# Optimization experiments

Hardware: AMD Instinct MI355X
Metric: run time of the kernel (lower is better)

Reference implementation:

```python
import jax, jax.numpy as jnp
import numpy as np
from jax.ops import segment_sum, segment_max

B, P, NP, EP = 128, 16, 256, 1280
EPG, ODIM, NH = 2048, 256, 128
EPS = 1e-5


def _bn(x, g, b):
    # BatchNorm1d (training-mode batch statistics), biased variance like torch
    mu = x.mean(0)
    var = ((x - mu) ** 2).mean(0)
    return g * (x - mu) * jax.lax.rsqrt(var + EPS) + b


def _gat(feat, src, dst, W, al, ar, resW, bias):
    # DGL GATConv: fc -> per-head attn logits -> leaky_relu -> edge softmax over dst -> aggregate; + residual fc + bias
    n = feat.shape[0]
    H, D = al.shape
    z = (feat @ W).reshape(n, H, D)
    el = (z * al).sum(-1)                                  # [n,H]
    er = (z * ar).sum(-1)
    e = jax.nn.leaky_relu(el[src] + er[dst], 0.2)          # [E,H]
    m = segment_max(e, dst, num_segments=n)
    ex = jnp.exp(e - m[dst])
    s = segment_sum(ex, dst, num_segments=n)
    a = ex / (s[dst] + 1e-9)
    rst = segment_sum(a[:, :, None] * z[src], dst, num_segments=n)  # [n,H,D]
    res = (feat @ resW).reshape(n, H, D)
    return (rst + res + bias.reshape(1, H, D)).reshape(n, H * D)


def _plane(feat, src, dst, p):
    # PlaneGraphEncoder forward (eval: dropout off)
    h = _gat(feat, src, dst, p['W1'], p['al1'], p['ar1'], p['res1'], p['b1'])
    h = jax.nn.relu(_bn(h, p['g1'], p['be1']))
    h = _gat(h, src, dst, p['W2'], p['al2'], p['ar2'], p['res2'], p['b2'])
    h = jax.nn.relu(_bn(h, p['g2'], p['be2']))
    rep = h.mean(0)                                        # dgl.mean_nodes -> [32]
    d = jax.nn.relu(_bn(h @ p['dW1'] + p['db1'], p['dg'], p['dbe']))
    recon = d @ p['dW2'] + p['db2']                        # [n,1]
    rloss = jnp.mean((recon - feat) ** 2)
    return rep, rloss


def _masked_gc(h, src, dst, mask_f, W, b):
    # DGL GraphConv(norm='both') with edge_weight = mask[src]*mask[dst]; structural degrees, clamp>=1
    n = h.shape[0]
    ones = jnp.ones(src.shape[0], h.dtype)
    d_out = jnp.maximum(segment_sum(ones, src, num_segments=n), 1.0)
    d_in = jnp.maximum(segment_sum(ones, dst, num_segments=n), 1.0)
    ew = mask_f[src] * mask_f[dst]                         # [E]
    hs = h * jax.lax.rsqrt(d_out)[:, None]
    agg = segment_sum(ew[:, None] * hs[src], dst, num_segments=n)
    return (agg * jax.lax.rsqrt(d_in)[:, None]) @ W + b


def _forward(plane_feat, original_features,
             W1, al1, ar1, res1, b1, g1, be1,
             W2, al2, ar2, res2, b2, g2, be2,
             dW1, db1, dg, dbe, dW2, db2,
             ft_W, ft_b, ft_g, ft_be, gc_W, gc_b, gbn_g, gbn_be,
             c1_W, c1_b, ln_g, ln_be, c2_W, c2_b,
             plane_src, plane_dst, patient_src, patient_dst, mask):
    pp = dict(W1=W1, al1=al1, ar1=ar1, res1=res1, b1=b1, g1=g1, be1=be1,
              W2=W2, al2=al2, ar2=ar2, res2=res2, b2=b2, g2=g2, be2=be2,
              dW1=dW1, db1=db1, dg=dg, dbe=dbe, dW2=dW2, db2=db2)
    enc_b = jax.vmap(_plane, in_axes=(0, 0, 0, None))      # over patients
    enc_pb = jax.vmap(enc_b, in_axes=(1, 1, 1, 0))         # over planes (params axis 0)
    reps, rlosses = enc_pb(plane_feat, plane_src, plane_dst, pp)   # [P,B,32], [P,B]
    plane_rep = jnp.transpose(reps, (1, 0, 2)).reshape(plane_feat.shape[0], -1)  # [B, P*32]
    avg_recon = rlosses.mean()                             # sum / (B*P)

    x = jnp.concatenate([original_features, plane_rep], axis=1)   # [B, fused]
    h = jax.nn.relu(_bn(x @ ft_W + ft_b, ft_g, ft_be))
    mask_f = mask.astype(h.dtype)
    h_sum = h
    for i in range(3):
        hn = _masked_gc(h, patient_src, patient_dst, mask_f, gc_W[i], gc_b[i])
        hn = jax.nn.relu(_bn(hn, gbn_g[i], gbn_be[i]))
        h = hn + h
        h_sum = h_sum + h
    h = h_sum / 4.0                                        # mean over [h0,h1,h2,h3]

    z = h @ c1_W + c1_b
    mu = z.mean(-1, keepdims=True)
    var = ((z - mu) ** 2).mean(-1, keepdims=True)
    z = jax.nn.relu(ln_g * (z - mu) * jax.lax.rsqrt(var + EPS) + ln_be)
    logits = z @ c2_W + c2_b
    return logits, avg_recon


def setup_inputs() -> dict:
    key = jax.random.key(0)
    ks = iter(jax.random.split(key, 64))
    f = lambda shape, s=0.1: jax.random.normal(next(ks), shape, jnp.float32) * s
    inp = dict(
        plane_feat=f((B, P, NP, 1), 1.0),
        plane_src=jax.random.randint(next(ks), (B, P, EP), 0, NP, jnp.int32),
        plane_dst=jax.random.randint(next(ks), (B, P, EP), 0, NP, jnp.int32),
        patient_src=jax.random.randint(next(ks), (EPG,), 0, B, jnp.int32),
        patient_dst=jax.random.randint(next(ks), (EPG,), 0, B, jnp.int32),
        original_features=f((B, ODIM), 1.0),
        mask=jax.random.randint(next(ks), (B,), 0, 2, jnp.int32),
        # per-plane encoder params, stacked over P
        W1=f((P, 1, 128)), al1=f((P, 2, 64)), ar1=f((P, 2, 64)),
        res1=f((P, 1, 128)), b1=f((P, 128)),
        g1=jnp.ones((P, 128)), be1=jnp.zeros((P, 128)),
        W2=f((P, 128, 32)), al2=f((P, 1, 32)), ar2=f((P, 1, 32)),
        res2=f((P, 128, 32)), b2=f((P, 32)),
        g2=jnp.ones((P, 32)), be2=jnp.zeros((P, 32)),
        dW1=f((P, 32, 128)), db1=f((P, 128)),
        dg=jnp.ones((P, 128)), dbe=jnp.zeros((P, 128)),
        dW2=f((P, 128, 1)), db2=f((P, 1)),
        # patient-level params
        ft_W=f((ODIM + P * 32, NH)), ft_b=f((NH,)),
        ft_g=jnp.ones((NH,)), ft_be=jnp.zeros((NH,)),
        gc_W=f((3, NH, NH)), gc_b=f((3, NH)),
        gbn_g=jnp.ones((3, NH)), gbn_be=jnp.zeros((3, NH)),
        c1_W=f((NH, NH // 2)), c1_b=f((NH // 2,)),
        ln_g=jnp.ones((NH // 2,)), ln_be=jnp.zeros((NH // 2,)),
        c2_W=f((NH // 2, 2)), c2_b=f((2,)),
    )
    return inp


def reference(plane_feat, plane_src, plane_dst, patient_src, patient_dst,
              original_features, mask,
              W1, al1, ar1, res1, b1, g1, be1,
              W2, al2, ar2, res2, b2, g2, be2,
              dW1, db1, dg, dbe, dW2, db2,
              ft_W, ft_b, ft_g, ft_be, gc_W, gc_b, gbn_g, gbn_be,
              c1_W, c1_b, ln_g, ln_be, c2_W, c2_b):
    return _forward(plane_feat, original_features,
                    W1, al1, ar1, res1, b1, g1, be1,
                    W2, al2, ar2, res2, b2, g2, be2,
                    dW1, db1, dg, dbe, dW2, db2,
                    ft_W, ft_b, ft_g, ft_be, gc_W, gc_b, gbn_g, gbn_be,
                    c1_W, c1_b, ln_g, ln_be, c2_W, c2_b,
                    plane_src, plane_dst, patient_src, patient_dst, mask)
```

## Files before the change

### kernel.cpp

```cpp
#include <hip/hip_runtime.h>

#define B_    128
#define P_    16
#define NP_   256
#define EP_   1280
#define EPG_  2048
#define ODIM_ 256
#define NH_   128

typedef __attribute__((ext_vector_type(8))) short s8_t;
typedef __attribute__((ext_vector_type(4))) short s4_t;
typedef __attribute__((ext_vector_type(4))) float f4_t;

__device__ __forceinline__ unsigned short f2b(float x) {
  unsigned u = __builtin_bit_cast(unsigned, x);
  u = (u + 0x7fffu + ((u >> 16) & 1u)) >> 16;
  return (unsigned short)u;
}
__device__ __forceinline__ float b2f(short x) {
  unsigned u = ((unsigned)(unsigned short)x) << 16;
  return __builtin_bit_cast(float, u);
}

struct SmemA {
  float f[256];
  union {
    __align__(16) unsigned short wT1[64 * 136];
    __align__(16) unsigned short z2[256 * 40];
  } u1;
  __align__(16) unsigned short dW1T[128 * 36];
  union {
    struct { float S0a[256]; float S1a[256]; } a;
    float redf[512];
  } u2;
  float el2[256], er2[256];
  union {
    struct { float abg0[128], abg1[128], abg2[128]; } a;
    struct { float al2v[32], ar2v[32], dW2v[128]; } b;
  } u3;
  union {
    int cnt[256];
    struct { float scA[32], shA[32], dscA[64], dshA[64]; } b;
  } u4;
  unsigned short esrc[1280];
  int wtot[4];
  float r8[4][8]; float stat[8]; float wA[2], wB[2];
  float rlacc;
};

__global__ __launch_bounds__(256, 3) void plane_enc(
    const float* __restrict__ feat, const int* __restrict__ esrcg, const int* __restrict__ edstg,
    const float* __restrict__ W1, const float* __restrict__ al1, const float* __restrict__ ar1,
    const float* __restrict__ res1, const float* __restrict__ b1, const float* __restrict__ g1,
    const float* __restrict__ be1,
    const float* __restrict__ W2, const float* __restrict__ al2, const float* __restrict__ ar2,
    const float* __restrict__ res2, const float* __restrict__ g2, const float* __restrict__ be2,
    const float* __restrict__ dW1, const float* __restrict__ dg, const float* __restrict__ dbe,
    const float* __restrict__ dW2, const float* __restrict__ db2,
    float* __restrict__ rep_out, float* __restrict__ rlp_out)
{
  __shared__ SmemA s;
  const int g = blockIdx.x;
  const int p = g & 15;
  const int t = threadIdx.x;
  const int lane = t & 63, wv = t >> 6;
  const int l15 = lane & 15, quad = lane >> 4;

  s.f[t] = feat[g * NP_ + t];
  if (t == 0) s.rlacc = 0.f;
  s.u4.cnt[t] = 0;
  __syncthreads();

  const int* gs = esrcg + g * EP_;
  const int* gd = edstg + g * EP_;
  for (int k = t; k < EP_; k += 256) atomicAdd(&s.u4.cnt[gd[k]], 1);
  __syncthreads();
  int v = s.u4.cnt[t];
  int incl = v;
  #pragma unroll
  for (int off = 1; off < 64; off <<= 1) {
    int n = __shfl_up(incl, off, 64);
    if (lane >= off) incl += n;
  }
  if (lane == 63) s.wtot[wv] = incl;
  __syncthreads();
  int woff = 0;
  for (int w = 0; w < wv; w++) woff += s.wtot[w];
  const int myStart = woff + incl - v;
  const int myDeg = v;
  __syncthreads();
  s.u4.cnt[t] = myStart;
  __syncthreads();
  for (int k = t; k < EP_; k += 256) {
    int d = gd[k];
    int pos = atomicAdd(&s.u4.cnt[d], 1);
    s.esrc[pos] = (unsigned short)gs[k];
  }
  {
    const float* W2g = W2 + p * 4096;
    const float* Rg  = res2 + p * 4096;
    for (int q = 0; q < 16; q++) {
      int idx = t + 256 * q;
      int k = idx >> 5, n = idx & 31;
      s.u1.wT1[n * 136 + k]        = f2b(W2g[idx]);
      s.u1.wT1[(n + 32) * 136 + k] = f2b(Rg[idx]);
    }
  }
  if (t < 128) {
    float w1v = W1[p * 128 + t];
    s.el2[t] = w1v * al1[p * 128 + t];
    s.er2[t] = w1v * ar1[p * 128 + t];
  }
  __syncthreads();
  if (t < 2) {
    float a = 0.f, bq = 0.f;
    for (int d2 = 0; d2 < 64; d2++) { a += s.el2[t * 64 + d2]; bq += s.er2[t * 64 + d2]; }
    s.wA[t] = a; s.wB[t] = bq;
  }
  __syncthreads();

  const float fi = s.f[t];
  float S0, S1;
  {
    const float wa0 = s.wA[0], wb0 = s.wB[0], wa1 = s.wA[1], wb1 = s.wB[1];
    float m0 = -1e30f, m1 = -1e30f;
    for (int j = 0; j < myDeg; j++) {
      float fs = s.f[s.esrc[myStart + j]];
      float e0 = wa0 * fs + wb0 * fi; e0 = e0 > 0.f ? e0 : 0.2f * e0;
      float e1 = wa1 * fs + wb1 * fi; e1 = e1 > 0.f ? e1 : 0.2f * e1;
      m0 = fmaxf(m0, e0); m1 = fmaxf(m1, e1);
    }
    float ss0 = 0.f, ss1 = 0.f, U0 = 0.f, U1 = 0.f;
    for (int j = 0; j < myDeg; j++) {
      float fs = s.f[s.esrc[myStart + j]];
      float e0 = wa0 * fs + wb0 * fi; e0 = e0 > 0.f ? e0 : 0.2f * e0;
      float e1 = wa1 * fs + wb1 * fi; e1 = e1 > 0.f ? e1 : 0.2f * e1;
      float x0 = __expf(e0 - m0), x1 = __expf(e1 - m1);
      ss0 += x0; U0 += x0 * fs;
      ss1 += x1; U1 += x1 * fs;
    }
    S0 = U0 / (ss0 + 1e-9f);
    S1 = U1 / (ss1 + 1e-9f);
    s.u2.a.S0a[t] = S0; s.u2.a.S1a[t] = S1;
  }

  {
    float vals[8] = {fi, fi * fi, S0, S0 * S0, S0 * fi, S1, S1 * S1, S1 * fi};
    #pragma unroll
    for (int d2 = 32; d2 > 0; d2 >>= 1) {
      #pragma unroll
      for (int q = 0; q < 8; q++) vals[q] += __shfl_down(vals[q], d2, 64);
    }
    if (lane == 0) {
      #pragma unroll
      for (int q = 0; q < 8; q++) s.r8[wv][q] = vals[q];
    }
  }
  __syncthreads();
  if (t < 8) s.stat[t] = (s.r8[0][t] + s.r8[1][t] + s.r8[2][t] + s.r8[3][t]) * (1.f / 256.f);
  __syncthreads();
  if (t < 128) {
    float mf = s.stat[0], ef2 = s.stat[1];
    int hh = t >> 6;
    float mS = s.stat[2 + 3 * hh], eS2 = s.stat[3 + 3 * hh], eSf = s.stat[4 + 3 * hh];
    float varS = eS2 - mS * mS, varf = ef2 - mf * mf, cov = eSf - mS * mf;
    float Wv = W1[p * 128 + t], Rv = res1[p * 128 + t], Bv = b1[p * 128 + t];
    float mu  = Wv * mS + Rv * mf + Bv;
    float var = Wv * Wv * varS + Rv * Rv * varf + 2.f * Wv * Rv * cov;
    float gn  = g1[p * 128 + t] * rsqrtf(var + 1e-5f);
    s.u3.a.abg0[t] = gn * Wv;
    s.u3.a.abg1[t] = gn * Rv;
    s.u3.a.abg2[t] = gn * (Bv - mu) + be1[p * 128 + t];
  }
  __syncthreads();

  float resv[32];
  {
    f4_t accum[4][4];
    #pragma unroll
    for (int i = 0; i < 4; i++)
      #pragma unroll
      for (int nt = 0; nt < 4; nt++) accum[i][nt] = (f4_t){0.f, 0.f, 0.f, 0.f};

    float fm[4], s0m[4], s1m[4];
    #pragma unroll
    for (int i = 0; i < 4; i++) {
      int m = (wv * 4 + i) * 16 + l15;
      fm[i] = s.f[m]; s0m[i] = s.u2.a.S0a[m]; s1m[i] = s.u2.a.S1a[m];
    }
    #pragma unroll
    for (int kt = 0; kt < 4; kt++) {
      int cbase = kt * 32 + quad * 8;
      float a0[8], a1[8], a2[8];
      #pragma unroll
      for (int j = 0; j < 8; j++) {
        a0[j] = s.u3.a.abg0[cbase + j]; a1[j] = s.u3.a.abg1[cbase + j]; a2[j] = s.u3.a.abg2[cbase + j];
      }
      s8_t afr[4];
      #pragma unroll
      for (int i = 0; i < 4; i++) {
        float Sm = (kt < 2) ? s0m[i] : s1m[i];
        union { s8_t v; unsigned short u[8]; } fu;
        #pragma unroll
        for (int j = 0; j < 8; j++) {
          float h = fmaxf(fmaf(a0[j], Sm, fmaf(a1[j], fm[i], a2[j])), 0.f);
          fu.u[j] = f2b(h);
        }
        afr[i] = fu.v;
      }
      s8_t bfr[4];
      #pragma unroll
      for (int nt = 0; nt < 4; nt++)
        bfr[nt] = *(const s8_t*)&s.u1.wT1[(nt * 16 + l15) * 136 + cbase];
      #pragma unroll
      for (int i = 0; i < 4; i++)
        #pragma unroll
        for (int nt = 0; nt < 4; nt++)
          accum[i][nt] = __builtin_amdgcn_mfma_f32_16x16x32_bf16(afr[i], bfr[nt], accum[i][nt], 0, 0, 0);
    }
    __syncthreads();
    #pragma unroll
    for (int i = 0; i < 4; i++) {
      int mBase = (wv * 4 + i) * 16 + quad * 4;
      #pragma unroll
      for (int nt = 0; nt < 2; nt++) {
        int col = nt * 16 + l15;
        #pragma unroll
        for (int r = 0; r < 4; r++)
          s.u1.z2[(mBase + r) * 40 + col] = f2b(accum[i][nt][r]);
      }
      #pragma unroll
      for (int h2 = 0; h2 < 2; h2++)
        #pragma unroll
        for (int r = 0; r < 4; r++)
          resv[(i * 2 + h2) * 4 + r] = accum[i][2 + h2][r];
    }
  }
  if (t < 32) { s.u3.b.al2v[t] = al2[p * 32 + t]; s.u3.b.ar2v[t] = ar2[p * 32 + t]; }
  if (t < 128) s.u3.b.dW2v[t] = dW2[p * 128 + t];
  {
    const float* Dg = dW1 + p * 4096;
    #pragma unroll
    for (int q = 0; q < 16; q++) {
      int idx = t + 256 * q;
      int k = idx >> 7, n = idx & 127;
      s.dW1T[n * 36 + k] = f2b(Dg[idx]);
    }
  }
  const float db2v = db2[p];
  __syncthreads();

  {
    const s8_t* zr = (const s8_t*)&s.u1.z2[t * 40];
    float el = 0.f, er = 0.f;
    #pragma unroll
    for (int q = 0; q < 4; q++) {
      s8_t vz = zr[q];
      #pragma unroll
      for (int j = 0; j < 8; j++) {
        float zv = b2f(vz[j]);
        el += zv * s.u3.b.al2v[q * 8 + j];
        er += zv * s.u3.b.ar2v[q * 8 + j];
      }
    }
    s.el2[t] = el; s.er2[t] = er;
  }
  __syncthreads();

  float hrow[32];
  {
    const float eri = s.er2[t];
    float m = -1e30f;
    for (int j = 0; j < myDeg; j++) {
      float e = s.el2[s.esrc[myStart + j]] + eri;
      e = e > 0.f ? e : 0.2f * e;
      m = fmaxf(m, e);
    }
    float ss = 0.f;
    #pragma unroll
    for (int d2 = 0; d2 < 32; d2++) hrow[d2] = 0.f;
    for (int j = 0; j < myDeg; j++) {
      int sj = s.esrc[myStart + j];
      float e = s.el2[sj] + eri;
      e = e > 0.f ? e : 0.2f * e;
      float x = __expf(e - m);
      ss += x;
      const s8_t* zr = (const s8_t*)&s.u1.z2[sj * 40];
      #pragma unroll
      for (int q = 0; q < 4; q++) {
        s8_t vz = zr[q];
        #pragma unroll
        for (int jj = 0; jj < 8; jj++) hrow[q * 8 + jj] += x * b2f(vz[jj]);
      }
    }
    float inv = 1.f / (ss + 1e-9f);
    #pragma unroll
    for (int d2 = 0; d2 < 32; d2++) hrow[d2] *= inv;
  }
  __syncthreads();
  #pragma unroll
  for (int i = 0; i < 4; i++) {
    int mBase = (wv * 4 + i) * 16 + quad * 4;
    #pragma unroll
    for (int h2 = 0; h2 < 2; h2++) {
      int col = h2 * 16 + l15;
      #pragma unroll
      for (int r = 0; r < 4; r++)
        s.u1.z2[(mBase + r) * 40 + col] = f2b(resv[(i * 2 + h2) * 4 + r]);
    }
  }
  __syncthreads();
  {
    const s8_t* zr = (const s8_t*)&s.u1.z2[t * 40];
    #pragma unroll
    for (int q = 0; q < 4; q++) {
      s8_t vz = zr[q];
      #pragma unroll
      for (int jj = 0; jj < 8; jj++) hrow[q * 8 + jj] += b2f(vz[jj]);
    }
  }
  #pragma unroll
  for (int d2 = 0; d2 < 32; d2++) s.u1.z2[t * 40 + d2] = f2b(hrow[d2]);
  __syncthreads();

  {
    int c = t & 31, gq = t >> 5;
    float s1 = 0.f, s2 = 0.f;
    for (int j = 0; j < 32; j++) {
      float vz = b2f((short)s.u1.z2[(gq * 32 + j) * 40 + c]);
      s1 += vz; s2 += vz * vz;
    }
    s.u2.redf[t] = s1; s.u2.redf[256 + t] = s2;
  }
  __syncthreads();
  if (t < 32) {
    float s1 = 0.f, s2 = 0.f;
    #pragma unroll
    for (int q = 0; q < 8; q++) { s1 += s.u2.redf[q * 32 + t]; s2 += s.u2.redf[256 + q * 32 + t]; }
    float mu = s1 * (1.f / 256.f);
    float var = s2 * (1.f / 256.f) - mu * mu;
    float a = g2[p * 32 + t] * rsqrtf(var + 1e-5f);
    s.u4.b.scA[t] = a; s.u4.b.shA[t] = be2[p * 32 + t] - a * mu;
  }
  __syncthreads();
  {
    int c = t & 31, gq = t >> 5;
    float a = s.u4.b.scA[c], bb = s.u4.b.shA[c];
    float s1 = 0.f;
    for (int j = 0; j < 32; j++) {
      int ad = (gq * 32 + j) * 40 + c;
      float vz = b2f((short)s.u1.z2[ad]);
      float hv = fmaxf(a * vz + bb, 0.f);
      s.u1.z2[ad] = f2b(hv);
      s1 += hv;
    }
    s.u2.redf[t] = s1;
  }
  __syncthreads();
  if (t < 32) {
    float s1 = 0.f;
    #pragma unroll
    for (int q = 0; q < 8; q++) s1 += s.u2.redf[q * 32 + t];
    rep_out[g * 32 + t] = s1 * (1.f / 256.f);
  }
  __syncthreads();

  {
    s8_t afr2[4];
    #pragma unroll
    for (int i = 0; i < 4; i++)
      afr2[i] = *(const s8_t*)&s.u1.z2[((wv * 4 + i) * 16 + l15) * 40 + quad * 8];
    float rAcc[4][4];
    #pragma unroll
    for (int i = 0; i < 4; i++)
      #pragma unroll
      for (int r = 0; r < 4; r++) rAcc[i][r] = 0.f;

    for (int half = 0; half < 2; half++) {
      __syncthreads();
      s.u2.redf[t] = 0.f; s.u2.redf[256 + t] = 0.f;
      __syncthreads();
      f4_t acc2[4][4];
      #pragma unroll
      for (int i = 0; i < 4; i++)
        #pragma unroll
        for (int nt = 0; nt < 4; nt++) acc2[i][nt] = (f4_t){0.f, 0.f, 0.f, 0.f};
      s8_t bfr[4];
      #pragma unroll
      for (int nt = 0; nt < 4; nt++) {
        const s4_t* pr = (const s4_t*)&s.dW1T[(half * 64 + nt * 16 + l15) * 36 + quad * 8];
        s4_t lo = pr[0], hi = pr[1];
        bfr[nt] = __builtin_shufflevector(lo, hi, 0, 1, 2, 3, 4, 5, 6, 7);
      }
      #pragma unroll
      for (int i = 0; i < 4; i++)
        #pragma unroll
        for (int nt = 0; nt < 4; nt++)
          acc2[i][nt] = __builtin_amdgcn_mfma_f32_16x16x32_bf16(afr2[i], bfr[nt], acc2[i][nt], 0, 0, 0);
      #pragma unroll
      for (int nt = 0; nt < 4; nt++) {
        float s1 = 0.f, s2 = 0.f;
        #pragma unroll
        for (int i = 0; i < 4; i++)
          #pragma unroll
          for (int r = 0; r < 4; r++) { float vv = acc2[i][nt][r]; s1 += vv; s2 += vv * vv; }
        atomicAdd(&s.u2.redf[nt * 16 + l15], s1);
        atomicAdd(&s.u2.redf[256 + nt * 16 + l15], s2);
      }
      __syncthreads();
      if (t < 64) {
        int col = half * 64 + t;
        float mu = s.u2.redf[t] * (1.f / 256.f);
        float var = s.u2.redf[256 + t] * (1.f / 256.f) - mu * mu;
        float a = dg[p * 128 + col] * rsqrtf(var + 1e-5f);
        s.u4.b.dscA[t] = a; s.u4.b.dshA[t] = dbe[p * 128 + col] - a * mu;
      }
      __syncthreads();
      #pragma unroll
      for (int nt = 0; nt < 4; nt++) {
        int cl = nt * 16 + l15;
        float a = s.u4.b.dscA[cl], bb = s.u4.b.dshA[cl], w2 = s.u3.b.dW2v[half * 64 + cl];
        #pragma unroll
        for (int i = 0; i < 4; i++)
          #pragma unroll
          for (int r = 0; r < 4; r++) {
            float dv = fmaxf(a * acc2[i][nt][r] + bb, 0.f);
            rAcc[i][r] += dv * w2;
          }
      }
    }
    #pragma unroll
    for (int off = 1; off < 16; off <<= 1)
      #pragma unroll
      for (int i = 0; i < 4; i++)
        #pragma unroll
        for (int r = 0; r < 4; r++) rAcc[i][r] += __shfl_xor(rAcc[i][r], off, 64);
    if (l15 == 0) {
      float sq = 0.f;
      #pragma unroll
      for (int i = 0; i < 4; i++)
        #pragma unroll
        for (int r = 0; r < 4; r++) {
          int m = (wv * 4 + i) * 16 + quad * 4 + r;
          float diff = rAcc[i][r] + db2v - s.f[m];
          sq += diff * diff;
        }
      atomicAdd(&s.rlacc, sq);
    }
  }
  __syncthreads();
  if (t == 0) rlp_out[g] = s.rlacc;
}

__global__ __launch_bounds__(256) void ft_mm(
    const float* __restrict__ orig, const float* __restrict__ rep,
    const float* __restrict__ ftW, float* __restrict__ hpre,
    const int* __restrict__ ps, const int* __restrict__ pd,
    const int* __restrict__ mask, unsigned short* __restrict__ abar)
{
  const int t = threadIdx.x;

  if (blockIdx.x == 8) {
    __shared__ int aB[128 * 128];
    __shared__ int co[128], ci[128];
    __shared__ float facs[128], facd[128];
    for (int idx = t; idx < 16384; idx += 256) aB[idx] = 0;
    if (t < 128) { co[t] = 0; ci[t] = 0; }
    __syncthreads();
    for (int e = t; e < EPG_; e += 256) {
      int sN = ps[e], d = pd[e];
      atomicAdd(&co[sN], 1);
      atomicAdd(&ci[d], 1);
      atomicAdd(&aB[d * 128 + sN], 1);
    }
    __syncthreads();
    if (t < 128) {
      float mk = (float)mask[t];
      int da = co[t] > 1 ? co[t] : 1;
      int db = ci[t] > 1 ? ci[t] : 1;
      facs[t] = mk * rsqrtf((float)da);
      facd[t] = mk * rsqrtf((float)db);
    }
    __syncthreads();
    for (int idx = t; idx < 16384; idx += 256) {
      int d = idx >> 7, sN = idx & 127;
      abar[idx] = f2b((float)aB[idx] * facd[d] * facs[sN]);
    }
    return;
  }

  const int wv = t >> 6, lane = t & 63;
  const int l15 = lane & 15, quad = lane >> 4;
  const int m = blockIdx.x * 16 + l15;

  f4_t acc[2];
  acc[0] = (f4_t){0.f, 0.f, 0.f, 0.f};
  acc[1] = (f4_t){0.f, 0.f, 0.f, 0.f};
  for (int kt = 0; kt < 24; kt++) {
    int k0 = kt * 32 + quad * 8;
    const float* px = (k0 < 256) ? (orig + m * 256 + k0) : (rep + m * 512 + (k0 - 256));
    float4 xa = ((const float4*)px)[0];
    float4 xb = ((const float4*)px)[1];
    union { s8_t v; unsigned short u[8]; } fu;
    fu.u[0] = f2b(xa.x); fu.u[1] = f2b(xa.y); fu.u[2] = f2b(xa.z); fu.u[3] = f2b(xa.w);
    fu.u[4] = f2b(xb.x); fu.u[5] = f2b(xb.y); fu.u[6] = f2b(xb.z); fu.u[7] = f2b(xb.w);
    #pragma unroll
    for (int nt = 0; nt < 2; nt++) {
      int col = wv * 32 + nt * 16 + l15;
      union { s8_t v; unsigned short u[8]; } bu;
      #pragma unroll
      for (int j = 0; j < 8; j++) bu.u[j] = f2b(ftW[(k0 + j) * 128 + col]);
      acc[nt] = __builtin_amdgcn_mfma_f32_16x16x32_bf16(fu.v, bu.v, acc[nt], 0, 0, 0);
    }
  }
  #pragma unroll
  for (int nt = 0; nt < 2; nt++) {
    int col = wv * 32 + nt * 16 + l15;
    #pragma unroll
    for (int r = 0; r < 4; r++)
      hpre[(blockIdx.x * 16 + quad * 4 + r) * 128 + col] = acc[nt][r];
  }
}

struct SmemB {
  __align__(16) unsigned short arow[128 * 136];
  __align__(16) unsigned short hT[128 * 136];
  union {
    struct {
      union {
        __align__(16) unsigned short wT[128 * 136];
        float zF[128 * 68];
      } w;
      __align__(16) unsigned short aggB[128 * 136];
    } mm;
  } u;
  float redA[1024], redB[1024];
  float scB[128], shB[128];
};

__global__ __launch_bounds__(1024) void k_patient(
    const float* __restrict__ hpre, const unsigned short* __restrict__ abar,
    const float* __restrict__ ftg, const float* __restrict__ ftbe,
    const float* __restrict__ gcW, const float* __restrict__ gbng, const float* __restrict__ gbnbe,
    const float* __restrict__ c1W, const float* __restrict__ c1b,
    const float* __restrict__ lng, const float* __restrict__ lnbe,
    const float* __restrict__ c2W, const float* __restrict__ c2b,
    const float* __restrict__ rlp, float* __restrict__ out)
{
  __shared__ SmemB s;
  const int t = threadIdx.x;
  const int w = t >> 6, lane = t & 63;
  const int l15 = lane & 15, quad = lane >> 4;
  const int mb = w & 7, nb = (w >> 3) * 64;

  for (int idx = t; idx < 16384; idx += 1024) {
    int d = idx >> 7, sN = idx & 127;
    s.arow[d * 136 + sN] = abar[idx];
  }

  f4_t acc[4];
  #pragma unroll
  for (int nt = 0; nt < 4; nt++) {
    int col = nb + nt * 16 + l15;
    #pragma unroll
    for (int r = 0; r < 4; r++)
      acc[nt][r] = hpre[(mb * 16 + quad * 4 + r) * 128 + col];
  }

  float hR[16], hsumR[16];
  {
    #pragma unroll
    for (int nt = 0; nt < 4; nt++) {
      float s1 = acc[nt][0] + acc[nt][1] + acc[nt][2] + acc[nt][3];
      float s2 = acc[nt][0]*acc[nt][0] + acc[nt][1]*acc[nt][1] + acc[nt][2]*acc[nt][2] + acc[nt][3]*acc[nt][3];
      s1 += __shfl_xor(s1, 16, 64); s1 += __shfl_xor(s1, 32, 64);
      s2 += __shfl_xor(s2, 16, 64); s2 += __shfl_xor(s2, 32, 64);
      if (quad == 0) {
        s.redA[mb * 128 + nb + nt * 16 + l15] = s1;
        s.redB[mb * 128 + nb + nt * 16 + l15] = s2;
      }
    }
    __syncthreads();
    if (t < 128) {
      float a1 = 0.f, a2 = 0.f;
      #pragma unroll
      for (int q = 0; q < 8; q++) { a1 += s.redA[q * 128 + t]; a2 += s.redB[q * 128 + t]; }
      float mu = a1 * (1.f / 128.f), var = a2 * (1.f / 128.f) - mu * mu;
      float a = ftg[t] * rsqrtf(var + 1e-5f);
      s.scB[t] = a; s.shB[t] = ftbe[t] - a * mu;
    }
    __syncthreads();
    #pragma unroll
    for (int nt = 0; nt < 4; nt++) {
      int col = nb + nt * 16 + l15;
      float a = s.scB[col], bb = s.shB[col];
      #pragma unroll
      for (int r = 0; r < 4; r++) {
        int row = mb * 16 + quad * 4 + r;
        float hv = fmaxf(a * acc[nt][r] + bb, 0.f);
        hR[nt * 4 + r] = hv; hsumR[nt * 4 + r] = hv;
        s.hT[col * 136 + row] = f2b(hv);
      }
    }
  }
  __syncthreads();

  for (int layer = 0; layer < 3; layer++) {
    #pragma unroll
    for (int q = 0; q < 16; q++) {
      int idx = t + 1024 * q;
      int kk = idx >> 7, n = idx & 127;
      s.u.mm.w.wT[n * 136 + kk] = f2b(gcW[layer * 16384 + kk * 128 + n]);
    }
    f4_t ag[4];
    #pragma unroll
    for (int nt = 0; nt < 4; nt++) ag[nt] = (f4_t){0.f, 0.f, 0.f, 0.f};
    #pragma unroll
    for (int ks = 0; ks < 4; ks++) {
      s8_t afr = *(const s8_t*)&s.arow[(mb * 16 + l15) * 136 + ks * 32 + quad * 8];
      #pragma unroll
      for (int nt = 0; nt < 4; nt++) {
        s8_t bfr = *(const s8_t*)&s.hT[(nb + nt * 16 + l15) * 136 + ks * 32 + quad * 8];
        ag[nt] = __builtin_amdgcn_mfma_f32_16x16x32_bf16(afr, bfr, ag[nt], 0, 0, 0);
      }
    }
    #pragma unroll
    for (int nt = 0; nt < 4; nt++) {
      int col = nb + nt * 16 + l15;
      #pragma unroll
      for (int r = 0; r < 4; r++)
        s.u.mm.aggB[(mb * 16 + quad * 4 + r) * 136 + col] = f2b(ag[nt][r]);
    }
    __syncthreads();
    f4_t oc[4];
    #pragma unroll
    for (int nt = 0; nt < 4; nt++) oc[nt] = (f4_t){0.f, 0.f, 0.f, 0.f};
    #pragma unroll
    for (int ks = 0; ks < 4; ks++) {
      s8_t afr = *(const s8_t*)&s.u.mm.aggB[(mb * 16 + l15) * 136 + ks * 32 + quad * 8];
      #pragma unroll
      for (int nt = 0; nt < 4; nt++) {
        s8_t bfr = *(const s8_t*)&s.u.mm.w.wT[(nb + nt * 16 + l15) * 136 + ks * 32 + quad * 8];
        oc[nt] = __builtin_amdgcn_mfma_f32_16x16x32_bf16(afr, bfr, oc[nt], 0, 0, 0);
      }
    }
    #pragma unroll
    for (int nt = 0; nt < 4; nt++) {
      float s1 = oc[nt][0] + oc[nt][1] + oc[nt][2] + oc[nt][3];
      float s2 = oc[nt][0]*oc[nt][0] + oc[nt][1]*oc[nt][1] + oc[nt][2]*oc[nt][2] + oc[nt][3]*oc[nt][3];
      s1 += __shfl_xor(s1, 16, 64); s1 += __shfl_xor(s1, 32, 64);
      s2 += __shfl_xor(s2, 16, 64); s2 += __shfl_xor(s2, 32, 64);
      if (quad == 0) {
        s.redA[mb * 128 + nb + nt * 16 + l15] = s1;
        s.redB[mb * 128 + nb + nt * 16 + l15] = s2;
      }
    }
    __syncthreads();
    if (t < 128) {
      float a1 = 0.f, a2 = 0.f;
      #pragma unroll
      for (int q = 0; q < 8; q++) { a1 += s.redA[q * 128 + t]; a2 += s.redB[q * 128 + t]; }
      float mu = a1 * (1.f / 128.f), var = a2 * (1.f / 128.f) - mu * mu;
      float a = gbng[layer * 128 + t] * rsqrtf(var + 1e-5f);
      s.scB[t] = a; s.shB[t] = gbnbe[layer * 128 + t] - a * mu;
    }
    __syncthreads();
    #pragma unroll
    for (int nt = 0; nt < 4; nt++) {
      int col = nb + nt * 16 + l15;
      float a = s.scB[col], bb = s.shB[col];
      #pragma unroll
      for (int r = 0; r < 4; r++) {
        int row = mb * 16 + quad * 4 + r;
        float hn = fmaxf(a * oc[nt][r] + bb, 0.f) + hR[nt * 4 + r];
        hR[nt * 4 + r] = hn;
        hsumR[nt * 4 + r] += hn;
        s.hT[col * 136 + row] = f2b(hn);
      }
    }
    __syncthreads();
  }

  #pragma unroll
  for (int nt = 0; nt < 4; nt++) {
    int col = nb + nt * 16 + l15;
    #pragma unroll
    for (int r = 0; r < 4; r++)
      s.u.mm.aggB[(mb * 16 + quad * 4 + r) * 136 + col] = f2b(hsumR[nt * 4 + r] * 0.25f);
  }
  #pragma unroll
  for (int q = 0; q < 8; q++) {
    int idx = t + 1024 * q;
    int n = idx & 63, kk = idx >> 6;
    s.u.mm.w.wT[n * 136 + kk] = f2b(c1W[kk * 64 + n]);
  }
  __syncthreads();
  {
    const int nb2 = (w >> 3) * 32;
    f4_t zc[2];
    #pragma unroll
    for (int nt = 0; nt < 2; nt++) zc[nt] = (f4_t){0.f, 0.f, 0.f, 0.f};
    #pragma unroll
    for (int ks = 0; ks < 4; ks++) {
      s8_t afr = *(const s8_t*)&s.u.mm.aggB[(mb * 16 + l15) * 136 + ks * 32 + quad * 8];
      #pragma unroll
      for (int nt = 0; nt < 2; nt++) {
        s8_t bfr = *(const s8_t*)&s.u.mm.w.wT[(nb2 + nt * 16 + l15) * 136 + ks * 32 + quad * 8];
        zc[nt] = __builtin_amdgcn_mfma_f32_16x16x32_bf16(afr, bfr, zc[nt], 0, 0, 0);
      }
    }
    __syncthreads();
    #pragma unroll
    for (int nt = 0; nt < 2; nt++) {
      int col = nb2 + nt * 16 + l15;
      #pragma unroll
      for (int r = 0; r < 4; r++)
        s.u.mm.w.zF[(mb * 16 + quad * 4 + r) * 68 + col] = zc[nt][r] + c1b[col];
    }
  }
  __syncthreads();
  if (t < 128) {
    float s1 = 0.f, s2 = 0.f;
    #pragma unroll
    for (int j = 0; j < 64; j++) { float zv = s.u.mm.w.zF[t * 68 + j]; s1 += zv; s2 += zv * zv; }
    float mu = s1 * (1.f / 64.f);
    float var = s2 * (1.f / 64.f) - mu * mu;
    float rs = rsqrtf(var + 1e-5f);
    float l0 = 0.f, l1 = 0.f;
    #pragma unroll
    for (int j = 0; j < 64; j++) {
      float zv = s.u.mm.w.zF[t * 68 + j];
      float zn = fmaxf(lng[j] * (zv - mu) * rs + lnbe[j], 0.f);
      l0 += zn * c2W[j * 2];
      l1 += zn * c2W[j * 2 + 1];
    }
    out[t * 2]     = l0 + c2b[0];
    out[t * 2 + 1] = l1 + c2b[1];
  }

  {
    float r = rlp[t] + rlp[t + 1024];
    #pragma unroll
    for (int off = 32; off > 0; off >>= 1) r += __shfl_down(r, off, 64);
    if (lane == 0) s.redA[w] = r;
  }
  __syncthreads();
  if (t == 0) {
    float tot = 0.f;
    #pragma unroll
    for (int i = 0; i < 16; i++) tot += s.redA[i];
    out[256] = tot * (1.f / (256.f * 2048.f));
  }
}

extern "C" void kernel_launch(void* const* d_in, const int* in_sizes, int n_in,
                              void* d_out, int out_size, void* d_ws, size_t ws_size,
                              hipStream_t stream) {
  (void)in_sizes; (void)n_in; (void)out_size; (void)ws_size;
  const float* plane_feat  = (const float*)d_in[0];
  const int*   plane_src   = (const int*)d_in[1];
  const int*   plane_dst   = (const int*)d_in[2];
  const int*   patient_src = (const int*)d_in[3];
  const int*   patient_dst = (const int*)d_in[4];
  const float* orig        = (const float*)d_in[5];
  const int*   mask        = (const int*)d_in[6];
  const float* W1   = (const float*)d_in[7];
  const float* al1  = (const float*)d_in[8];
  const float* ar1  = (const float*)d_in[9];
  const float* res1 = (const float*)d_in[10];
  const float* b1   = (const float*)d_in[11];
  const float* g1   = (const float*)d_in[12];
  const float* be1  = (const float*)d_in[13];
  const float* W2   = (const float*)d_in[14];
  const float* al2  = (const float*)d_in[15];
  const float* ar2  = (const float*)d_in[16];
  const float* res2 = (const float*)d_in[17];
  const float* g2   = (const float*)d_in[19];
  const float* be2  = (const float*)d_in[20];
  const float* dW1  = (const float*)d_in[21];
  const float* dg   = (const float*)d_in[23];
  const float* dbe  = (const float*)d_in[24];
  const float* dW2  = (const float*)d_in[25];
  const float* db2  = (const float*)d_in[26];
  const float* ftW  = (const float*)d_in[27];
  const float* ftg  = (const float*)d_in[29];
  const float* ftbe = (const float*)d_in[30];
  const float* gcW  = (const float*)d_in[31];
  const float* gbng = (const float*)d_in[33];
  const float* gbnbe= (const float*)d_in[34];
  const float* c1W  = (const float*)d_in[35];
  const float* c1b  = (const float*)d_in[36];
  const float* lng  = (const float*)d_in[37];
  const float* lnbe = (const float*)d_in[38];
  const float* c2W  = (const float*)d_in[39];
  const float* c2b  = (const float*)d_in[40];

  float* ws   = (float*)d_ws;
  float* rep  = ws;
  float* hpre = ws + 65536;
  unsigned short* abar = (unsigned short*)(ws + 81920);
  float* rlp  = ws + 90112;
  float* outp = (float*)d_out;

  plane_enc<<<2048, 256, 0, stream>>>(plane_feat, plane_src, plane_dst,
      W1, al1, ar1, res1, b1, g1, be1, W2, al2, ar2, res2, g2, be2,
      dW1, dg, dbe, dW2, db2, rep, rlp);
  ft_mm<<<9, 256, 0, stream>>>(orig, rep, ftW, hpre,
      patient_src, patient_dst, mask, abar);
  k_patient<<<1, 1024, 0, stream>>>(hpre, abar, ftg, ftbe,
      gcW, gbng, gbnbe, c1W, c1b, lng, lnbe, c2W, c2b, rlp, outp);
}
```

Baseline: 318.9 us.

## Cut register pressure in plane encoder to raise occupancy to four blocks per CU

Raises the launch bound from 3 to 4 blocks per CU and restructures the kernel to fit the smaller per-thread register budget. The residual GEMM is split from the z GEMM and its result kept packed as bf16 pairs. GAT aggregation now runs in two 16-column halves, so it walks the edge list twice. The decoder MFMA is also recomputed in two groups instead of being held in registers. The aim is more waves per CU to hide latency, at the cost of extra MFMA work, extra edge passes and earlier bf16 rounding of the residual.

```diff
diff --git a/kernel.cpp b/kernel.cpp
--- a/kernel.cpp
+++ b/kernel.cpp
@@ -48,7 +48,7 @@
   float rlacc;
 };
 
-__global__ __launch_bounds__(256, 3) void plane_enc(
+__global__ __launch_bounds__(256, 4) void plane_enc(
     const float* __restrict__ feat, const int* __restrict__ esrcg, const int* __restrict__ edstg,
     const float* __restrict__ W1, const float* __restrict__ al1, const float* __restrict__ ar1,
     const float* __restrict__ res1, const float* __restrict__ b1, const float* __restrict__ g1,
@@ -174,20 +174,60 @@
   }
   __syncthreads();
 
-  float resv[32];
-  {
-    f4_t accum[4][4];
-    #pragma unroll
-    for (int i = 0; i < 4; i++)
-      #pragma unroll
-      for (int nt = 0; nt < 4; nt++) accum[i][nt] = (f4_t){0.f, 0.f, 0.f, 0.f};
-
+  unsigned resvP[16];
+  f4_t accz[4][2];
+  {
     float fm[4], s0m[4], s1m[4];
     #pragma unroll
     for (int i = 0; i < 4; i++) {
       int m = (wv * 4 + i) * 16 + l15;
       fm[i] = s.f[m]; s0m[i] = s.u2.a.S0a[m]; s1m[i] = s.u2.a.S1a[m];
     }
+    {
+      f4_t accr[4][2];
+      #pragma unroll
+      for (int i = 0; i < 4; i++) { accr[i][0] = (f4_t){0,0,0,0}; accr[i][1] = (f4_t){0,0,0,0}; }
+      #pragma unroll
+      for (int kt = 0; kt < 4; kt++) {
+        int cbase = kt * 32 + quad * 8;
+        float a0[8], a1[8], a2[8];
+        #pragma unroll
+        for (int j = 0; j < 8; j++) {
+          a0[j] = s.u3.a.abg0[cbase + j]; a1[j] = s.u3.a.abg1[cbase + j]; a2[j] = s.u3.a.abg2[cbase + j];
+        }
+        s8_t afr[4];
+        #pragma unroll
+        for (int i = 0; i < 4; i++) {
+          float Sm = (kt < 2) ? s0m[i] : s1m[i];
+          union { s8_t v; unsigned short u[8]; } fu;
+          #pragma unroll
+          for (int j = 0; j < 8; j++) {
+            float h = fmaxf(fmaf(a0[j], Sm, fmaf(a1[j], fm[i], a2[j])), 0.f);
+            fu.u[j] = f2b(h);
+          }
+          afr[i] = fu.v;
+        }
+        s8_t bfr0 = *(const s8_t*)&s.u1.wT1[(2 * 16 + l15) * 136 + cbase];
+        s8_t bfr1 = *(const s8_t*)&s.u1.wT1[(3 * 16 + l15) * 136 + cbase];
+        #pragma unroll
+        for (int i = 0; i < 4; i++) {
+          accr[i][0] = __builtin_amdgcn_mfma_f32_16x16x32_bf16(afr[i], bfr0, accr[i][0], 0, 0, 0);
+          accr[i][1] = __builtin_amdgcn_mfma_f32_16x16x32_bf16(afr[i], bfr1, accr[i][1], 0, 0, 0);
+        }
+      }
+      #pragma unroll
+      for (int i = 0; i < 4; i++)
+        #pragma unroll
+        for (int h2 = 0; h2 < 2; h2++)
+          #pragma unroll
+          for (int rp = 0; rp < 2; rp++) {
+            unsigned lo = f2b(accr[i][h2][rp * 2]);
+            unsigned hi = f2b(accr[i][h2][rp * 2 + 1]);
+            resvP[(i * 2 + h2) * 2 + rp] = lo | (hi << 16);
+          }
+    }
+    #pragma unroll
+    for (int i = 0; i < 4; i++) { accz[i][0] = (f4_t){0,0,0,0}; accz[i][1] = (f4_t){0,0,0,0}; }
     #pragma unroll
     for (int kt = 0; kt < 4; kt++) {
       int cbase = kt * 32 + quad * 8;
@@ -208,32 +248,25 @@
         }
         afr[i] = fu.v;
       }
-      s8_t bfr[4];
-      #pragma unroll
-      for (int nt = 0; nt < 4; nt++)
-        bfr[nt] = *(const s8_t*)&s.u1.wT1[(nt * 16 + l15) * 136 + cbase];
-      #pragma unroll
-      for (int i = 0; i < 4; i++)
-        #pragma unroll
-        for (int nt = 0; nt < 4; nt++)
-          accum[i][nt] = __builtin_amdgcn_mfma_f32_16x16x32_bf16(afr[i], bfr[nt], accum[i][nt], 0, 0, 0);
-    }
-    __syncthreads();
-    #pragma unroll
-    for (int i = 0; i < 4; i++) {
-      int mBase = (wv * 4 + i) * 16 + quad * 4;
-      #pragma unroll
-      for (int nt = 0; nt < 2; nt++) {
-        int col = nt * 16 + l15;
-        #pragma unroll
-        for (int r = 0; r < 4; r++)
-          s.u1.z2[(mBase + r) * 40 + col] = f2b(accum[i][nt][r]);
-      }
-      #pragma unroll
-      for (int h2 = 0; h2 < 2; h2++)
-        #pragma unroll
-        for (int r = 0; r < 4; r++)
-          resv[(i * 2 + h2) * 4 + r] = accum[i][2 + h2][r];
+      s8_t bfr0 = *(const s8_t*)&s.u1.wT1[(l15) * 136 + cbase];
+      s8_t bfr1 = *(const s8_t*)&s.u1.wT1[(16 + l15) * 136 + cbase];
+      #pragma unroll
+      for (int i = 0; i < 4; i++) {
+        accz[i][0] = __builtin_amdgcn_mfma_f32_16x16x32_bf16(afr[i], bfr0, accz[i][0], 0, 0, 0);
+        accz[i][1] = __builtin_amdgcn_mfma_f32_16x16x32_bf16(afr[i], bfr1, accz[i][1], 0, 0, 0);
+      }
+    }
+  }
+  __syncthreads();
+  #pragma unroll
+  for (int i = 0; i < 4; i++) {
+    int mBase = (wv * 4 + i) * 16 + quad * 4;
+    #pragma unroll
+    for (int nt = 0; nt < 2; nt++) {
+      int col = nt * 16 + l15;
+      #pragma unroll
+      for (int r = 0; r < 4; r++)
+        s.u1.z2[(mBase + r) * 40 + col] = f2b(accz[i][nt][r]);
     }
   }
   if (t < 32) { s.u3.b.al2v[t] = al2[p * 32 + t]; s.u3.b.ar2v[t] = ar2[p * 32 + t]; }
@@ -267,7 +300,6 @@
   }
   __syncthreads();
 
-  float hrow[32];
   {
     const float eri = s.er2[t];
     float m = -1e30f;
@@ -276,9 +308,10 @@
       e = e > 0.f ? e : 0.2f * e;
       m = fmaxf(m, e);
     }
+    float hrow[16];
     float ss = 0.f;
     #pragma unroll
-    for (int d2 = 0; d2 < 32; d2++) hrow[d2] = 0.f;
+    for (int d2 = 0; d2 < 16; d2++) hrow[d2] = 0.f;
     for (int j = 0; j < myDeg; j++) {
       int sj = s.esrc[myStart + j];
       float e = s.el2[sj] + eri;
@@ -287,40 +320,73 @@
       ss += x;
       const s8_t* zr = (const s8_t*)&s.u1.z2[sj * 40];
       #pragma unroll
-      for (int q = 0; q < 4; q++) {
+      for (int q = 0; q < 2; q++) {
         s8_t vz = zr[q];
         #pragma unroll
         for (int jj = 0; jj < 8; jj++) hrow[q * 8 + jj] += x * b2f(vz[jj]);
       }
     }
-    float inv = 1.f / (ss + 1e-9f);
-    #pragma unroll
-    for (int d2 = 0; d2 < 32; d2++) hrow[d2] *= inv;
-  }
-  __syncthreads();
-  #pragma unroll
-  for (int i = 0; i < 4; i++) {
-    int mBase = (wv * 4 + i) * 16 + quad * 4;
-    #pragma unroll
-    for (int h2 = 0; h2 < 2; h2++) {
-      int col = h2 * 16 + l15;
+    const float inv = 1.f / (ss + 1e-9f);
+    __syncthreads();
+    #pragma unroll
+    for (int i = 0; i < 4; i++) {
+      int mBase = (wv * 4 + i) * 16 + quad * 4;
       #pragma unroll
       for (int r = 0; r < 4; r++)
-        s.u1.z2[(mBase + r) * 40 + col] = f2b(resv[(i * 2 + h2) * 4 + r]);
-    }
-  }
-  __syncthreads();
-  {
-    const s8_t* zr = (const s8_t*)&s.u1.z2[t * 40];
-    #pragma unroll
-    for (int q = 0; q < 4; q++) {
-      s8_t vz = zr[q];
-      #pragma unroll
-      for (int jj = 0; jj < 8; jj++) hrow[q * 8 + jj] += b2f(vz[jj]);
-    }
-  }
-  #pragma unroll
-  for (int d2 = 0; d2 < 32; d2++) s.u1.z2[t * 40 + d2] = f2b(hrow[d2]);
+        s.u1.z2[(mBase + r) * 40 + l15] =
+            (unsigned short)(resvP[i * 4 + (r >> 1)] >> ((r & 1) * 16));
+    }
+    __syncthreads();
+    {
+      const s8_t* zr = (const s8_t*)&s.u1.z2[t * 40];
+      #pragma unroll
+      for (int q = 0; q < 2; q++) {
+        s8_t vz = zr[q];
+        #pragma unroll
+        for (int jj = 0; jj < 8; jj++)
+          hrow[q * 8 + jj] = fmaf(hrow[q * 8 + jj], inv, b2f(vz[jj]));
+      }
+      #pragma unroll
+      for (int d2 = 0; d2 < 16; d2++) s.u1.z2[t * 40 + d2] = f2b(hrow[d2]);
+    }
+    #pragma unroll
+    for (int d2 = 0; d2 < 16; d2++) hrow[d2] = 0.f;
+    for (int j = 0; j < myDeg; j++) {
+      int sj = s.esrc[myStart + j];
+      float e = s.el2[sj] + eri;
+      e = e > 0.f ? e : 0.2f * e;
+      float x = __expf(e - m);
+      const s8_t* zr = (const s8_t*)&s.u1.z2[sj * 40];
+      #pragma unroll
+      for (int q = 0; q < 2; q++) {
+        s8_t vz = zr[2 + q];
+        #pragma unroll
+        for (int jj = 0; jj < 8; jj++) hrow[q * 8 + jj] += x * b2f(vz[jj]);
+      }
+    }
+    __syncthreads();
+    #pragma unroll
+    for (int i = 0; i < 4; i++) {
+      int mBase = (wv * 4 + i) * 16 + quad * 4;
+      #pragma unroll
+      for (int r = 0; r < 4; r++)
+        s.u1.z2[(mBase + r) * 40 + 16 + l15] =
+            (unsigned short)(resvP[(i * 2 + 1) * 2 + (r >> 1)] >> ((r & 1) * 16));
+    }
+    __syncthreads();
+    {
+      const s8_t* zr = (const s8_t*)&s.u1.z2[t * 40];
+      #pragma unroll
+      for (int q = 0; q < 2; q++) {
+        s8_t vz = zr[2 + q];
+        #pragma unroll
+        for (int jj = 0; jj < 8; jj++)
+          hrow[q * 8 + jj] = fmaf(hrow[q * 8 + jj], inv, b2f(vz[jj]));
+      }
+      #pragma unroll
+      for (int d2 = 0; d2 < 16; d2++) s.u1.z2[t * 40 + 16 + d2] = f2b(hrow[d2]);
+    }
+  }
   __syncthreads();
 
   {
@@ -380,32 +446,32 @@
       __syncthreads();
       s.u2.redf[t] = 0.f; s.u2.redf[256 + t] = 0.f;
       __syncthreads();
-      f4_t acc2[4][4];
-      #pragma unroll
-      for (int i = 0; i < 4; i++)
-        #pragma unroll
-        for (int nt = 0; nt < 4; nt++) acc2[i][nt] = (f4_t){0.f, 0.f, 0.f, 0.f};
-      s8_t bfr[4];
-      #pragma unroll
-      for (int nt = 0; nt < 4; nt++) {
-        const s4_t* pr = (const s4_t*)&s.dW1T[(half * 64 + nt * 16 + l15) * 36 + quad * 8];
-        s4_t lo = pr[0], hi = pr[1];
-        bfr[nt] = __builtin_shufflevector(lo, hi, 0, 1, 2, 3, 4, 5, 6, 7);
-      }
-      #pragma unroll
-      for (int i = 0; i < 4; i++)
-        #pragma unroll
-        for (int nt = 0; nt < 4; nt++)
-          acc2[i][nt] = __builtin_amdgcn_mfma_f32_16x16x32_bf16(afr2[i], bfr[nt], acc2[i][nt], 0, 0, 0);
-      #pragma unroll
-      for (int nt = 0; nt < 4; nt++) {
-        float s1 = 0.f, s2 = 0.f;
-        #pragma unroll
-        for (int i = 0; i < 4; i++)
+      #pragma unroll
+      for (int grp = 0; grp < 2; grp++) {
+        f4_t acc2[4][2];
+        #pragma unroll
+        for (int i = 0; i < 4; i++) { acc2[i][0] = (f4_t){0,0,0,0}; acc2[i][1] = (f4_t){0,0,0,0}; }
+        #pragma unroll
+        for (int ntl = 0; ntl < 2; ntl++) {
+          int nt = grp * 2 + ntl;
+          const s4_t* pr = (const s4_t*)&s.dW1T[(half * 64 + nt * 16 + l15) * 36 + quad * 8];
+          s4_t lo = pr[0], hi = pr[1];
+          s8_t bfr = __builtin_shufflevector(lo, hi, 0, 1, 2, 3, 4, 5, 6, 7);
           #pragma unroll
-          for (int r = 0; r < 4; r++) { float vv = acc2[i][nt][r]; s1 += vv; s2 += vv * vv; }
-        atomicAdd(&s.u2.redf[nt * 16 + l15], s1);
-        atomicAdd(&s.u2.redf[256 + nt * 16 + l15], s2);
+          for (int i = 0; i < 4; i++)
+            acc2[i][ntl] = __builtin_amdgcn_mfma_f32_16x16x32_bf16(afr2[i], bfr, acc2[i][ntl], 0, 0, 0);
+        }
+        #pragma unroll
+        for (int ntl = 0; ntl < 2; ntl++) {
+          int nt = grp * 2 + ntl;
+          float s1 = 0.f, s2 = 0.f;
+          #pragma unroll
+          for (int i = 0; i < 4; i++)
+            #pragma unroll
+            for (int r = 0; r < 4; r++) { float vv = acc2[i][ntl][r]; s1 += vv; s2 += vv * vv; }
+          atomicAdd(&s.u2.redf[nt * 16 + l15], s1);
+          atomicAdd(&s.u2.redf[256 + nt * 16 + l15], s2);
+        }
       }
       __syncthreads();
       if (t < 64) {
@@ -417,16 +483,32 @@
       }
       __syncthreads();
       #pragma unroll
-      for (int nt = 0; nt < 4; nt++) {
-        int cl = nt * 16 + l15;
-        float a = s.u4.b.dscA[cl], bb = s.u4.b.dshA[cl], w2 = s.u3.b.dW2v[half * 64 + cl];
-        #pragma unroll
-        for (int i = 0; i < 4; i++)
+      for (int grp = 0; grp < 2; grp++) {
+        f4_t acc2[4][2];
+        #pragma unroll
+        for (int i = 0; i < 4; i++) { acc2[i][0] = (f4_t){0,0,0,0}; acc2[i][1] = (f4_t){0,0,0,0}; }
+        #pragma unroll
+        for (int ntl = 0; ntl < 2; ntl++) {
+          int nt = grp * 2 + ntl;
+          const s4_t* pr = (const s4_t*)&s.dW1T[(half * 64 + nt * 16 + l15) * 36 + quad * 8];
+          s4_t lo = pr[0], hi = pr[1];
+          s8_t bfr = __builtin_shufflevector(lo, hi, 0, 1, 2, 3, 4, 5, 6, 7);
           #pragma unroll
-          for (int r = 0; r < 4; r++) {
-            float dv = fmaxf(a * acc2[i][nt][r] + bb, 0.f);
-            rAcc[i][r] += dv * w2;
-          }
+          for (int i = 0; i < 4; i++)
+            acc2[i][ntl] = __builtin_amdgcn_mfma_f32_16x16x32_bf16(afr2[i], bfr, acc2[i][ntl], 0, 0, 0);
+        }
+        #pragma unroll
+        for (int ntl = 0; ntl < 2; ntl++) {
+          int cl = (grp * 2 + ntl) * 16 + l15;
+          float a = s.u4.b.dscA[cl], bb = s.u4.b.dshA[cl], w2 = s.u3.b.dW2v[half * 64 + cl];
+          #pragma unroll
+          for (int i = 0; i < 4; i++)
+            #pragma unroll
+            for (int r = 0; r < 4; r++) {
+              float dv = fmaxf(a * acc2[i][ntl][r] + bb, 0.f);
+              rAcc[i][r] += dv * w2;
+            }
+        }
       }
     }
     #pragma unroll
```

Measured after the change: 318.1 us. About the same (-0.2%).
